# Optimization experiments

Hardware: AMD Instinct MI355X
Metric: run time of the kernel (lower is better)

Reference implementation:

```python
import jax, jax.numpy as jnp
import numpy as np


def _reflect(x, size):
    # PyTorch grid_sample reflection padding, align_corners=False:
    # reflect about borders at -0.5 and size-0.5, then clip to [0, size-1].
    x = x + 0.5
    x = jnp.mod(x, 2.0 * size)
    x = jnp.where(x >= size, 2.0 * size - x, x)
    x = x - 0.5
    return jnp.clip(x, 0.0, size - 1.0)


def _grid_sample_one(img, grid):
    # img: (H, W, C); grid: (H, W, 2) with (x, y) in [-1, 1]
    H, W, _ = img.shape
    # unnormalize, align_corners=False
    ix = ((grid[..., 0] + 1.0) * W - 1.0) * 0.5
    iy = ((grid[..., 1] + 1.0) * H - 1.0) * 0.5
    ix = _reflect(ix, W)
    iy = _reflect(iy, H)
    x0 = jnp.floor(ix)
    y0 = jnp.floor(iy)
    wx = (ix - x0)[..., None]
    wy = (iy - y0)[..., None]
    x0i = jnp.clip(x0, 0, W - 1).astype(jnp.int32)
    x1i = jnp.clip(x0 + 1.0, 0, W - 1).astype(jnp.int32)
    y0i = jnp.clip(y0, 0, H - 1).astype(jnp.int32)
    y1i = jnp.clip(y0 + 1.0, 0, H - 1).astype(jnp.int32)
    Ia = img[y0i, x0i]  # (H, W, C)
    Ib = img[y0i, x1i]
    Ic = img[y1i, x0i]
    Id = img[y1i, x1i]
    return (Ia * (1 - wx) * (1 - wy) + Ib * wx * (1 - wy)
            + Ic * (1 - wx) * wy + Id * wx * wy)


def _displace(image, displacement_map, amplitude, angle):
    N, H, W, C = image.shape
    # base sampling grid, torch.linspace(-1, 1, size) endpoints included
    gy, gx = jnp.meshgrid(jnp.linspace(-1.0, 1.0, H, dtype=image.dtype),
                          jnp.linspace(-1.0, 1.0, W, dtype=image.dtype),
                          indexing='ij')
    base = jnp.stack([gx, gy], axis=-1)  # (H, W, 2) as (x, y)
    # bilinear resize (half-pixel centers == torch align_corners=False)
    dm = jax.image.resize(displacement_map,
                          (N, H, W, displacement_map.shape[-1]),
                          method='bilinear')
    if dm.shape[-1] == 3:
        dm = jnp.mean(dm, axis=-1)  # (N, H, W)
    else:
        dm = dm[..., 0]
    d = dm * amplitude[:, None, None]
    dx = jnp.cos(angle)[:, None, None] * d / (W - 1) * 2.0
    dy = jnp.sin(angle)[:, None, None] * d / (H - 1) * 2.0
    grid = base[None] + jnp.stack([dx, dy], axis=-1)  # (N, H, W, 2)
    return jax.vmap(_grid_sample_one)(image, grid)  # (N, H, W, C)


def setup_inputs() -> dict:
    key = jax.random.key(0)
    k1, k2, k3, k4 = jax.random.split(key, 4)
    N, H, W, C = 8, 1024, 1024, 3
    image = jax.random.normal(k1, (N, H, W, C), dtype=jnp.float32)
    displacement_map = jax.random.uniform(k2, (N, 512, 512, 3), dtype=jnp.float32)
    amplitude = jax.random.uniform(k3, (N,), dtype=jnp.float32) * 20.0  # pixels
    angle = jax.random.uniform(k4, (N,), dtype=jnp.float32) * 2.0 * np.pi
    return {"image": image, "displacement_map": displacement_map,
            "amplitude": amplitude, "angle": angle}


def reference(image, displacement_map, amplitude, angle):
    return _displace(image, displacement_map, amplitude, angle)
```

## Files before the change

### kernel.cpp

```cpp
#include <hip/hip_runtime.h>
#include <math.h>

__device__ __forceinline__ float reflect_coord(float x, float size) {
    x += 0.5f;
    float two = 2.0f * size;
    x = x - floorf(x / two) * two;
    if (x >= size) x = two - x;
    x -= 0.5f;
    return fminf(fmaxf(x, 0.0f), size - 1.0f);
}

__global__ __launch_bounds__(256) void displace_kernel(
    const float* __restrict__ img,
    const float* __restrict__ dmap,
    const float* __restrict__ amp,
    const float* __restrict__ ang,
    float* __restrict__ out,
    int N, int H, int W, int DH, int DW)
{
    long long idx = (long long)blockIdx.x * blockDim.x + threadIdx.x;
    long long total = (long long)N * H * W;
    if (idx >= total) return;

    int w = (int)(idx % W);
    long long t = idx / W;
    int h = (int)(t % H);
    int n = (int)(t / H);

    float sx = (w + 0.5f) * ((float)DW / (float)W) - 0.5f;
    float sy = (h + 0.5f) * ((float)DH / (float)H) - 0.5f;
    float fx = floorf(sx), fy = floorf(sy);
    float tx = sx - fx, ty = sy - fy;
    int dx0 = max(0, min(DW - 1, (int)fx));
    int dx1 = max(0, min(DW - 1, (int)fx + 1));
    int dy0 = max(0, min(DH - 1, (int)fy));
    int dy1 = max(0, min(DH - 1, (int)fy + 1));

    const float* dbase = dmap + (long long)n * DH * DW * 3;
    const float* p00 = dbase + ((long long)dy0 * DW + dx0) * 3;
    const float* p01 = dbase + ((long long)dy0 * DW + dx1) * 3;
    const float* p10 = dbase + ((long long)dy1 * DW + dx0) * 3;
    const float* p11 = dbase + ((long long)dy1 * DW + dx1) * 3;
    float m00 = p00[0] + p00[1] + p00[2];
    float m01 = p01[0] + p01[1] + p01[2];
    float m10 = p10[0] + p10[1] + p10[2];
    float m11 = p11[0] + p11[1] + p11[2];
    float dmv = ((m00 * (1.0f - tx) + m01 * tx) * (1.0f - ty)
               + (m10 * (1.0f - tx) + m11 * tx) * ty) * (1.0f / 3.0f);

    float a  = amp[n];
    float an = ang[n];
    float sa, ca;
    sincosf(an, &sa, &ca);
    float d   = dmv * a;
    float ddx = ca * d * (2.0f / (float)(W - 1));
    float ddy = sa * d * (2.0f / (float)(H - 1));

    float gx = -1.0f + 2.0f * (float)w / (float)(W - 1) + ddx;
    float gy = -1.0f + 2.0f * (float)h / (float)(H - 1) + ddy;

    float ix = ((gx + 1.0f) * (float)W - 1.0f) * 0.5f;
    float iy = ((gy + 1.0f) * (float)H - 1.0f) * 0.5f;
    ix = reflect_coord(ix, (float)W);
    iy = reflect_coord(iy, (float)H);

    float x0f = floorf(ix), y0f = floorf(iy);
    float wx = ix - x0f, wy = iy - y0f;
    int ix0 = min((int)x0f,     W - 1);
    int ix1 = min((int)x0f + 1, W - 1);
    int iy0 = min((int)y0f,     H - 1);
    int iy1 = min((int)y0f + 1, H - 1);

    const float* ibase = img + (long long)n * H * W * 3;
    const float* Ia = ibase + ((long long)iy0 * W + ix0) * 3;
    const float* Ib = ibase + ((long long)iy0 * W + ix1) * 3;
    const float* Ic = ibase + ((long long)iy1 * W + ix0) * 3;
    const float* Id = ibase + ((long long)iy1 * W + ix1) * 3;

    float wa = (1.0f - wx) * (1.0f - wy);
    float wb = wx * (1.0f - wy);
    float wc = (1.0f - wx) * wy;
    float wd = wx * wy;

    float* o = out + idx * 3;
    #pragma unroll
    for (int c = 0; c < 3; ++c) {
        o[c] = Ia[c] * wa + Ib[c] * wb + Ic[c] * wc + Id[c] * wd;
    }
}

extern "C" void kernel_launch(void* const* d_in, const int* in_sizes, int n_in,
                              void* d_out, int out_size, void* d_ws, size_t ws_size,
                              hipStream_t stream) {
    const float* img  = (const float*)d_in[0];
    const float* dmap = (const float*)d_in[1];
    const float* amp  = (const float*)d_in[2];
    const float* ang  = (const float*)d_in[3];
    float* out = (float*)d_out;

    int N = in_sizes[2];
    long long hw  = (long long)in_sizes[0] / ((long long)N * 3);
    int H = (int)llround(sqrt((double)hw));
    int W = H;
    long long dhw = (long long)in_sizes[1] / ((long long)N * 3);
    int DH = (int)llround(sqrt((double)dhw));
    int DW = DH;

    long long total = (long long)N * H * W;
    int block = 256;
    long long grid = (total + block - 1) / block;
    displace_kernel<<<(dim3)(unsigned)grid, block, 0, stream>>>(
        img, dmap, amp, ang, out, N, H, W, DH, DW);
}
```

Before: 221.5 us.

## Precompute channel-summed displacement map and per-batch scales, specialize main kernel

Splits the work into three kernels. A tiny kernel precomputes per-batch displacement scales (sincos times amplitude). A reduction kernel collapses the 3-channel displacement map to one channel, and a templated main kernel for 1024x1024/512x512 processes four pixels per thread with float4 output stores. This removes per-pixel redundant dmap channel loads, sincos and integer div/mod, and uses constexpr sizes. The cost is two extra launches and a workspace buffer; other shapes take a fallback path.

```diff
diff --git a/kernel.cpp b/kernel.cpp
--- a/kernel.cpp
+++ b/kernel.cpp
@@ -1,7 +1,134 @@
 #include <hip/hip_runtime.h>
 #include <math.h>
 
-__device__ __forceinline__ float reflect_coord(float x, float size) {
+__global__ void scales_kernel(const float* __restrict__ amp,
+                              const float* __restrict__ ang,
+                              float* __restrict__ sc,
+                              int N, float invW1, float invH1) {
+    int i = threadIdx.x;
+    if (i < N) {
+        float s, c;
+        sincosf(ang[i], &s, &c);
+        float a = amp[i] * (2.0f / 3.0f);
+        sc[2 * i]     = c * a * invW1;
+        sc[2 * i + 1] = s * a * invH1;
+    }
+}
+
+__global__ __launch_bounds__(256) void reduce_dmap_kernel(
+    const float* __restrict__ dmap, float* __restrict__ rd, long long npix) {
+    long long p0 = ((long long)blockIdx.x * blockDim.x + threadIdx.x) * 4;
+    if (p0 + 3 < npix) {
+        const float4* src = (const float4*)(dmap + p0 * 3);
+        float4 v0 = src[0], v1 = src[1], v2 = src[2];
+        float4 s;
+        s.x = v0.x + v0.y + v0.z;
+        s.y = v0.w + v1.x + v1.y;
+        s.z = v1.z + v1.w + v2.x;
+        s.w = v2.y + v2.z + v2.w;
+        *(float4*)(rd + p0) = s;
+    } else {
+        for (long long p = p0; p < npix; ++p) {
+            const float* s = dmap + p * 3;
+            rd[p] = s[0] + s[1] + s[2];
+        }
+    }
+}
+
+template <int S>
+__device__ __forceinline__ float reflectc(float x) {
+    x += 0.5f;
+    constexpr float two = 2.0f * S;
+    float q = floorf(x * (1.0f / two));
+    x = fmaf(-q, two, x);
+    if (x >= (float)S) x = two - x;
+    x -= 0.5f;
+    return fminf(fmaxf(x, 0.0f), (float)(S - 1));
+}
+
+template <int H, int W, int DH, int DW>
+__global__ __launch_bounds__(256) void displace_main(
+    const float* __restrict__ img,
+    const float* __restrict__ rd,
+    const float* __restrict__ sc,
+    float* __restrict__ out)
+{
+    const int n = blockIdx.z;
+    const int h = blockIdx.y;
+    const int w0 = ((int)blockIdx.x * (int)blockDim.x + (int)threadIdx.x) * 4;
+    if (w0 >= W) return;
+
+    constexpr float sDH = (float)DH / (float)H;
+    constexpr float sDW = (float)DW / (float)W;
+    float sy = fmaf((float)h + 0.5f, sDH, -0.5f);
+    float fy = floorf(sy);
+    float ty = sy - fy;
+    int iyf = (int)fy;
+    int dy0 = min(max(iyf, 0), DH - 1);
+    int dy1 = min(max(iyf + 1, 0), DH - 1);
+    const float* r0 = rd + ((long long)n * DH + dy0) * DW;
+    const float* r1 = rd + ((long long)n * DH + dy1) * DW;
+
+    const float scx = sc[2 * n];
+    const float scy = sc[2 * n + 1];
+    const float* ibase = img + (long long)n * H * W * 3;
+    const float gyb = fmaf((float)h, 2.0f / (float)(H - 1), -1.0f);
+
+    float acc[12];
+
+    #pragma unroll
+    for (int i = 0; i < 4; ++i) {
+        int w = w0 + i;
+        float sx = fmaf((float)w + 0.5f, sDW, -0.5f);
+        float fx = floorf(sx);
+        float tx = sx - fx;
+        int ixf = (int)fx;
+        int dx0 = min(max(ixf, 0), DW - 1);
+        int dx1 = min(max(ixf + 1, 0), DW - 1);
+        float a0 = r0[dx0], b0 = r0[dx1];
+        float a1 = r1[dx0], b1 = r1[dx1];
+        float m0 = fmaf(b0 - a0, tx, a0);
+        float m1 = fmaf(b1 - a1, tx, a1);
+        float ds = fmaf(m1 - m0, ty, m0);
+
+        float gx = fmaf((float)w, 2.0f / (float)(W - 1), -1.0f) + ds * scx;
+        float gy = gyb + ds * scy;
+
+        float ix = fmaf(gx + 1.0f, (float)W * 0.5f, -0.5f);
+        float iy = fmaf(gy + 1.0f, (float)H * 0.5f, -0.5f);
+        ix = reflectc<W>(ix);
+        iy = reflectc<H>(iy);
+
+        float x0f = floorf(ix), y0f = floorf(iy);
+        float wx = ix - x0f, wy = iy - y0f;
+        int ix0 = min((int)x0f, W - 1);
+        int ix1 = min((int)x0f + 1, W - 1);
+        int iy0 = min((int)y0f, H - 1);
+        int iy1 = min((int)y0f + 1, H - 1);
+
+        const float* Ia = ibase + ((long long)iy0 * W + ix0) * 3;
+        const float* Ib = ibase + ((long long)iy0 * W + ix1) * 3;
+        const float* Ic = ibase + ((long long)iy1 * W + ix0) * 3;
+        const float* Id = ibase + ((long long)iy1 * W + ix1) * 3;
+
+        float wa = (1.0f - wx) * (1.0f - wy);
+        float wb = wx * (1.0f - wy);
+        float wc = (1.0f - wx) * wy;
+        float wd = wx * wy;
+
+        #pragma unroll
+        for (int c = 0; c < 3; ++c) {
+            acc[3 * i + c] = Ia[c] * wa + Ib[c] * wb + Ic[c] * wc + Id[c] * wd;
+        }
+    }
+
+    float4* o = (float4*)(out + (((long long)n * H + h) * W + w0) * 3);
+    o[0] = make_float4(acc[0], acc[1], acc[2], acc[3]);
+    o[1] = make_float4(acc[4], acc[5], acc[6], acc[7]);
+    o[2] = make_float4(acc[8], acc[9], acc[10], acc[11]);
+}
+
+__device__ __forceinline__ float reflect_dyn(float x, float size) {
     x += 0.5f;
     float two = 2.0f * size;
     x = x - floorf(x / two) * two;
@@ -10,18 +137,14 @@
     return fminf(fmaxf(x, 0.0f), size - 1.0f);
 }
 
-__global__ __launch_bounds__(256) void displace_kernel(
-    const float* __restrict__ img,
-    const float* __restrict__ dmap,
-    const float* __restrict__ amp,
-    const float* __restrict__ ang,
-    float* __restrict__ out,
-    int N, int H, int W, int DH, int DW)
+__global__ __launch_bounds__(256) void displace_fallback(
+    const float* __restrict__ img, const float* __restrict__ dmap,
+    const float* __restrict__ amp, const float* __restrict__ ang,
+    float* __restrict__ out, int N, int H, int W, int DH, int DW)
 {
     long long idx = (long long)blockIdx.x * blockDim.x + threadIdx.x;
     long long total = (long long)N * H * W;
     if (idx >= total) return;
-
     int w = (int)(idx % W);
     long long t = idx / W;
     int h = (int)(t % H);
@@ -35,7 +158,6 @@
     int dx1 = max(0, min(DW - 1, (int)fx + 1));
     int dy0 = max(0, min(DH - 1, (int)fy));
     int dy1 = max(0, min(DH - 1, (int)fy + 1));
-
     const float* dbase = dmap + (long long)n * DH * DW * 3;
     const float* p00 = dbase + ((long long)dy0 * DW + dx0) * 3;
     const float* p01 = dbase + ((long long)dy0 * DW + dx1) * 3;
@@ -47,46 +169,34 @@
     float m11 = p11[0] + p11[1] + p11[2];
     float dmv = ((m00 * (1.0f - tx) + m01 * tx) * (1.0f - ty)
                + (m10 * (1.0f - tx) + m11 * tx) * ty) * (1.0f / 3.0f);
-
-    float a  = amp[n];
-    float an = ang[n];
-    float sa, ca;
+    float a = amp[n], an = ang[n], sa, ca;
     sincosf(an, &sa, &ca);
-    float d   = dmv * a;
-    float ddx = ca * d * (2.0f / (float)(W - 1));
-    float ddy = sa * d * (2.0f / (float)(H - 1));
-
-    float gx = -1.0f + 2.0f * (float)w / (float)(W - 1) + ddx;
-    float gy = -1.0f + 2.0f * (float)h / (float)(H - 1) + ddy;
-
+    float d = dmv * a;
+    float gx = -1.0f + 2.0f * (float)w / (float)(W - 1) + ca * d * (2.0f / (float)(W - 1));
+    float gy = -1.0f + 2.0f * (float)h / (float)(H - 1) + sa * d * (2.0f / (float)(H - 1));
     float ix = ((gx + 1.0f) * (float)W - 1.0f) * 0.5f;
     float iy = ((gy + 1.0f) * (float)H - 1.0f) * 0.5f;
-    ix = reflect_coord(ix, (float)W);
-    iy = reflect_coord(iy, (float)H);
-
+    ix = reflect_dyn(ix, (float)W);
+    iy = reflect_dyn(iy, (float)H);
     float x0f = floorf(ix), y0f = floorf(iy);
     float wx = ix - x0f, wy = iy - y0f;
-    int ix0 = min((int)x0f,     W - 1);
+    int ix0 = min((int)x0f, W - 1);
     int ix1 = min((int)x0f + 1, W - 1);
-    int iy0 = min((int)y0f,     H - 1);
+    int iy0 = min((int)y0f, H - 1);
     int iy1 = min((int)y0f + 1, H - 1);
-
     const float* ibase = img + (long long)n * H * W * 3;
     const float* Ia = ibase + ((long long)iy0 * W + ix0) * 3;
     const float* Ib = ibase + ((long long)iy0 * W + ix1) * 3;
     const float* Ic = ibase + ((long long)iy1 * W + ix0) * 3;
     const float* Id = ibase + ((long long)iy1 * W + ix1) * 3;
-
     float wa = (1.0f - wx) * (1.0f - wy);
     float wb = wx * (1.0f - wy);
     float wc = (1.0f - wx) * wy;
     float wd = wx * wy;
-
     float* o = out + idx * 3;
     #pragma unroll
-    for (int c = 0; c < 3; ++c) {
+    for (int c = 0; c < 3; ++c)
         o[c] = Ia[c] * wa + Ib[c] * wb + Ic[c] * wc + Id[c] * wd;
-    }
 }
 
 extern "C" void kernel_launch(void* const* d_in, const int* in_sizes, int n_in,
@@ -106,9 +216,28 @@
     int DH = (int)llround(sqrt((double)dhw));
     int DW = DH;
 
-    long long total = (long long)N * H * W;
-    int block = 256;
-    long long grid = (total + block - 1) / block;
-    displace_kernel<<<(dim3)(unsigned)grid, block, 0, stream>>>(
-        img, dmap, amp, ang, out, N, H, W, DH, DW);
-}
+    size_t need = 256 + (size_t)N * DH * DW * sizeof(float);
+
+    if (H == 1024 && W == 1024 && DH == 512 && DW == 512 && ws_size >= need) {
+        float* sc = (float*)d_ws;
+        float* rd = (float*)((char*)d_ws + 256);
+
+        scales_kernel<<<1, 64, 0, stream>>>(amp, ang, sc, N,
+                                            1.0f / (float)(W - 1),
+                                            1.0f / (float)(H - 1));
+
+        long long npix = (long long)N * DH * DW;
+        long long rthreads = (npix + 3) / 4;
+        int rgrid = (int)((rthreads + 255) / 256);
+        reduce_dmap_kernel<<<rgrid, 256, 0, stream>>>(dmap, rd, npix);
+
+        dim3 grid(W / (256 * 4), H, N);
+        displace_main<1024, 1024, 512, 512><<<grid, 256, 0, stream>>>(img, rd, sc, out);
+    } else {
+        long long total = (long long)N * H * W;
+        int block = 256;
+        long long grid = (total + block - 1) / block;
+        displace_fallback<<<(dim3)(unsigned)grid, block, 0, stream>>>(
+            img, dmap, amp, ang, out, N, H, W, DH, DW);
+    }
+}
```

Measured after the change: 312.7 us. 41.2% more time.

## Specialize displacement for 1024x1024 with channel-sum prepass and interleaved row order

Applied to the files above, without the earlier changes.

Adds a prep kernel that sums the three displacement-map channels into a workspace buffer and precomputes per-batch cosine and sine scale factors. A specialized main kernel then uses one 1024-thread block per output row, with constant-folded bilinear resize weights and a simplified reflection. It also interleaves rows across batch images in launch order. This is meant to cut displacement-map reads and index arithmetic in the memory-bound gather. The row interleave (lin&7) only maps rows correctly when N is 8, although the guard allows any N up to 256; other shapes use the original kernel as a fallback.

```diff
diff --git a/kernel.cpp b/kernel.cpp
--- a/kernel.cpp
+++ b/kernel.cpp
@@ -1,7 +1,88 @@
 #include <hip/hip_runtime.h>
 #include <math.h>
 
-__device__ __forceinline__ float reflect_coord(float x, float size) {
+__global__ __launch_bounds__(256) void prep_kernel(
+    const float* __restrict__ dmap, const float* __restrict__ amp,
+    const float* __restrict__ ang, float* __restrict__ sc,
+    float* __restrict__ rd, long long npix, int N, float fx, float fy) {
+    long long p = (long long)blockIdx.x * 256 + threadIdx.x;
+    if (p < npix) {
+        const float* s = dmap + p * 3;
+        rd[p] = s[0] + s[1] + s[2];
+    }
+    if (blockIdx.x == 0 && (int)threadIdx.x < N) {
+        int i = threadIdx.x;
+        float s_, c_;
+        sincosf(ang[i], &s_, &c_);
+        float a = amp[i] * (1.0f / 3.0f);
+        sc[2 * i]     = c_ * a * fx;
+        sc[2 * i + 1] = s_ * a * fy;
+    }
+}
+
+__global__ __launch_bounds__(1024, 8) void displace_main(
+    const float* __restrict__ img,
+    const float* __restrict__ rd,
+    const float* __restrict__ sc,
+    float* __restrict__ out)
+{
+    const int lin = (int)blockIdx.y * 1024 + (int)blockIdx.x;
+    const int hl  = (lin & 7) * 1024 + (lin >> 3);
+    const int n   = hl >> 10;
+    const int h   = hl & 1023;
+    const int w   = threadIdx.x;
+
+    const int dy0 = max((h - 1) >> 1, 0);
+    const int dy1 = min((h + 1) >> 1, 511);
+    const float ty = (h & 1) ? 0.25f : 0.75f;
+    const float* r0 = rd + (n * 512 + dy0) * 512;
+    const float* r1 = rd + (n * 512 + dy1) * 512;
+    const float scx = sc[2 * n];
+    const float scy = sc[2 * n + 1];
+    const float* ibase = img + (long long)n * (1024 * 1024 * 3);
+
+    const int dx0 = max((w - 1) >> 1, 0);
+    const int dx1 = min((w + 1) >> 1, 511);
+    const float tx = (w & 1) ? 0.25f : 0.75f;
+    float a0 = r0[dx0], b0 = r0[dx1];
+    float a1 = r1[dx0], b1 = r1[dx1];
+    float m0 = fmaf(b0 - a0, tx, a0);
+    float m1 = fmaf(b1 - a1, tx, a1);
+    float ds = fmaf(m1 - m0, ty, m0);
+
+    const float C = 1024.0f / 1023.0f;
+    float ux = fmaf((float)w, C, ds * scx);
+    float uy = fmaf((float)h, C, ds * scy);
+
+    ux = fabsf(ux); if (ux >= 1024.0f) ux = 2048.0f - ux;
+    uy = fabsf(uy); if (uy >= 1024.0f) uy = 2048.0f - uy;
+    float ix = fminf(fmaxf(ux - 0.5f, 0.0f), 1023.0f);
+    float iy = fminf(fmaxf(uy - 0.5f, 0.0f), 1023.0f);
+
+    int ix0 = (int)ix;
+    int iy0 = (int)iy;
+    float wx = ix - (float)ix0;
+    float wy = iy - (float)iy0;
+    int ix1 = min(ix0 + 1, 1023);
+    int iy1 = min(iy0 + 1, 1023);
+
+    const float* Ia = ibase + ((iy0 << 10) + ix0) * 3;
+    const float* Ib = ibase + ((iy0 << 10) + ix1) * 3;
+    const float* Ic = ibase + ((iy1 << 10) + ix0) * 3;
+    const float* Id = ibase + ((iy1 << 10) + ix1) * 3;
+
+    const float wa = (1.0f - wx) * (1.0f - wy);
+    const float wb = wx * (1.0f - wy);
+    const float wc = (1.0f - wx) * wy;
+    const float wd = wx * wy;
+
+    float* o = out + ((hl << 10) + w) * 3;
+    o[0] = Ia[0] * wa + Ib[0] * wb + Ic[0] * wc + Id[0] * wd;
+    o[1] = Ia[1] * wa + Ib[1] * wb + Ic[1] * wc + Id[1] * wd;
+    o[2] = Ia[2] * wa + Ib[2] * wb + Ic[2] * wc + Id[2] * wd;
+}
+
+__device__ __forceinline__ float reflect_dyn(float x, float size) {
     x += 0.5f;
     float two = 2.0f * size;
     x = x - floorf(x / two) * two;
@@ -10,18 +91,14 @@
     return fminf(fmaxf(x, 0.0f), size - 1.0f);
 }
 
-__global__ __launch_bounds__(256) void displace_kernel(
-    const float* __restrict__ img,
-    const float* __restrict__ dmap,
-    const float* __restrict__ amp,
-    const float* __restrict__ ang,
-    float* __restrict__ out,
-    int N, int H, int W, int DH, int DW)
+__global__ __launch_bounds__(256) void displace_fallback(
+    const float* __restrict__ img, const float* __restrict__ dmap,
+    const float* __restrict__ amp, const float* __restrict__ ang,
+    float* __restrict__ out, int N, int H, int W, int DH, int DW)
 {
     long long idx = (long long)blockIdx.x * blockDim.x + threadIdx.x;
     long long total = (long long)N * H * W;
     if (idx >= total) return;
-
     int w = (int)(idx % W);
     long long t = idx / W;
     int h = (int)(t % H);
@@ -35,7 +112,6 @@
     int dx1 = max(0, min(DW - 1, (int)fx + 1));
     int dy0 = max(0, min(DH - 1, (int)fy));
     int dy1 = max(0, min(DH - 1, (int)fy + 1));
-
     const float* dbase = dmap + (long long)n * DH * DW * 3;
     const float* p00 = dbase + ((long long)dy0 * DW + dx0) * 3;
     const float* p01 = dbase + ((long long)dy0 * DW + dx1) * 3;
@@ -47,46 +123,34 @@
     float m11 = p11[0] + p11[1] + p11[2];
     float dmv = ((m00 * (1.0f - tx) + m01 * tx) * (1.0f - ty)
                + (m10 * (1.0f - tx) + m11 * tx) * ty) * (1.0f / 3.0f);
-
-    float a  = amp[n];
-    float an = ang[n];
-    float sa, ca;
+    float a = amp[n], an = ang[n], sa, ca;
     sincosf(an, &sa, &ca);
-    float d   = dmv * a;
-    float ddx = ca * d * (2.0f / (float)(W - 1));
-    float ddy = sa * d * (2.0f / (float)(H - 1));
-
-    float gx = -1.0f + 2.0f * (float)w / (float)(W - 1) + ddx;
-    float gy = -1.0f + 2.0f * (float)h / (float)(H - 1) + ddy;
-
-    float ix = ((gx + 1.0f) * (float)W - 1.0f) * 0.5f;
-    float iy = ((gy + 1.0f) * (float)H - 1.0f) * 0.5f;
-    ix = reflect_coord(ix, (float)W);
-    iy = reflect_coord(iy, (float)H);
-
-    float x0f = floorf(ix), y0f = floorf(iy);
-    float wx = ix - x0f, wy = iy - y0f;
-    int ix0 = min((int)x0f,     W - 1);
+    float d = dmv * a;
+    float gx = -1.0f + 2.0f * (float)w / (float)(W - 1) + ca * d * (2.0f / (float)(W - 1));
+    float gy = -1.0f + 2.0f * (float)h / (float)(H - 1) + sa * d * (2.0f / (float)(H - 1));
+    float ixf2 = ((gx + 1.0f) * (float)W - 1.0f) * 0.5f;
+    float iyf2 = ((gy + 1.0f) * (float)H - 1.0f) * 0.5f;
+    ixf2 = reflect_dyn(ixf2, (float)W);
+    iyf2 = reflect_dyn(iyf2, (float)H);
+    float x0f = floorf(ixf2), y0f = floorf(iyf2);
+    float wx = ixf2 - x0f, wy = iyf2 - y0f;
+    int ix0 = min((int)x0f, W - 1);
     int ix1 = min((int)x0f + 1, W - 1);
-    int iy0 = min((int)y0f,     H - 1);
+    int iy0 = min((int)y0f, H - 1);
     int iy1 = min((int)y0f + 1, H - 1);
-
     const float* ibase = img + (long long)n * H * W * 3;
     const float* Ia = ibase + ((long long)iy0 * W + ix0) * 3;
     const float* Ib = ibase + ((long long)iy0 * W + ix1) * 3;
     const float* Ic = ibase + ((long long)iy1 * W + ix0) * 3;
     const float* Id = ibase + ((long long)iy1 * W + ix1) * 3;
-
     float wa = (1.0f - wx) * (1.0f - wy);
     float wb = wx * (1.0f - wy);
     float wc = (1.0f - wx) * wy;
     float wd = wx * wy;
-
     float* o = out + idx * 3;
     #pragma unroll
-    for (int c = 0; c < 3; ++c) {
+    for (int c = 0; c < 3; ++c)
         o[c] = Ia[c] * wa + Ib[c] * wb + Ic[c] * wc + Id[c] * wd;
-    }
 }
 
 extern "C" void kernel_launch(void* const* d_in, const int* in_sizes, int n_in,
@@ -106,9 +170,26 @@
     int DH = (int)llround(sqrt((double)dhw));
     int DW = DH;
 
-    long long total = (long long)N * H * W;
-    int block = 256;
-    long long grid = (total + block - 1) / block;
-    displace_kernel<<<(dim3)(unsigned)grid, block, 0, stream>>>(
-        img, dmap, amp, ang, out, N, H, W, DH, DW);
+    size_t need = 256 + (size_t)N * DH * DW * sizeof(float);
+
+    if (H == 1024 && W == 1024 && DH == 512 && DW == 512 && N <= 256 &&
+        ws_size >= need) {
+        float* sc = (float*)d_ws;
+        float* rd = (float*)((char*)d_ws + 256);
+
+        long long npix = (long long)N * DH * DW;
+        int pgrid = (int)((npix + 255) / 256);
+        prep_kernel<<<pgrid, 256, 0, stream>>>(
+            dmap, amp, ang, sc, rd, npix, N,
+            (float)W / (float)(W - 1), (float)H / (float)(H - 1));
+
+        dim3 grid(1024, (unsigned)N);
+        displace_main<<<grid, 1024, 0, stream>>>(img, rd, sc, out);
+    } else {
+        long long total = (long long)N * H * W;
+        int block = 256;
+        long long grid = (total + block - 1) / block;
+        displace_fallback<<<(dim3)(unsigned)grid, block, 0, stream>>>(
+            img, dmap, amp, ang, out, N, H, W, DH, DW);
+    }
 }
```

Result: slower. 242.8 us (+9.6%).
